# Kernel optimization log

Measured on AMD Instinct MI355X. Metric: run time of the kernel, lower is better.

The kernel has to match this reference:

```python
import jax, jax.numpy as jnp
import numpy as np
import math

N, LQ, C, HD, L, P = 2, 17821, 256, 8, 4, 4
D = C // HD
SHAPES = [(100, 134), (50, 67), (25, 34), (13, 17)]


def setup_inputs() -> dict:
    key = jax.random.key(0)
    ks = jax.random.split(key, 8)
    shapes = np.array(SHAPES, np.int32)
    areas = shapes[:, 0] * shapes[:, 1]
    starts = np.concatenate([[0], np.cumsum(areas)[:-1]]).astype(np.int32)
    Lin = int(areas.sum())
    sc = 1.0 / math.sqrt(C)
    # sampling_offsets bias: radial grid init as in _reset_parameters
    thetas = np.arange(HD, dtype=np.float32) * (2.0 * math.pi / HD)
    grid = np.stack([np.cos(thetas), np.sin(thetas)], -1)
    grid = grid / np.abs(grid).max(-1, keepdims=True)
    grid = np.tile(grid[:, None, None, :], (1, L, P, 1)) * np.arange(1, P + 1, dtype=np.float32)[None, None, :, None]
    boff = jnp.asarray(grid.reshape(-1), jnp.float32)
    return dict(
        query=jax.random.normal(ks[0], (N, LQ, C), jnp.float32),
        reference_points=jax.random.uniform(ks[1], (N, LQ, L, 2), jnp.float32),
        input_flatten=jax.random.normal(ks[2], (N, Lin, C), jnp.float32),
        input_spatial_shapes=jnp.asarray(shapes),
        input_level_start_index=jnp.asarray(starts),
        Wv=jax.random.normal(ks[3], (C, C), jnp.float32) * sc,
        bv=jnp.zeros((C,), jnp.float32),
        Woff=jax.random.normal(ks[4], (C, HD * L * P * 2), jnp.float32) * 0.01,
        boff=boff,
        Watt=jax.random.normal(ks[5], (C, HD * L * P), jnp.float32) * 0.02,
        batt=jnp.zeros((HD * L * P,), jnp.float32),
        Wout=jax.random.normal(ks[6], (C, C), jnp.float32) * sc,
        bout=jnp.zeros((C,), jnp.float32),
    )


def _ms_deform_attn_core(value, shapes, starts, loc, attw):
    # value: (N, Len_in, HD, D); loc: (N, Lq, HD, L, P, 2) in [0,1]; attw: (N, Lq, HD, L, P)
    n, lq = loc.shape[0], loc.shape[1]
    out = jnp.zeros((n, lq, HD, D), value.dtype)
    for l in range(L):
        H, W = int(shapes[l, 0]), int(shapes[l, 1])
        s = int(starts[l])
        v = value[:, s:s + H * W]                                    # (N, HW, HD, D)
        # (N,Lq,HD,P,2) -> (N,Lq,P,HD,2) -> (N,Lq*P,HD) per coord
        locl = loc[:, :, :, l].transpose(0, 1, 3, 2, 4).reshape(n, lq * P, HD, 2)
        # grid_sample align_corners=False mapping
        x = locl[..., 0] * W - 0.5
        y = locl[..., 1] * H - 0.5
        x0f, y0f = jnp.floor(x), jnp.floor(y)
        fx, fy = x - x0f, y - y0f
        x0, y0 = x0f.astype(jnp.int32), y0f.astype(jnp.int32)

        def corner(xi, yi, w):
            valid = (xi >= 0) & (xi < W) & (yi >= 0) & (yi < H)      # zero padding
            idx = jnp.clip(yi, 0, H - 1) * W + jnp.clip(xi, 0, W - 1)
            g = jnp.take_along_axis(v, idx[..., None], axis=1)        # (N, Lq*P, HD, D)
            return g * (w * valid)[..., None]

        samp = (corner(x0, y0, (1 - fx) * (1 - fy))
                + corner(x0 + 1, y0, fx * (1 - fy))
                + corner(x0, y0 + 1, (1 - fx) * fy)
                + corner(x0 + 1, y0 + 1, fx * fy))                    # (N, Lq*P, HD, D)
        aw = attw[:, :, :, l].transpose(0, 1, 3, 2).reshape(n, lq * P, HD)
        out = out + (samp * aw[..., None]).reshape(n, lq, P, HD, D).sum(axis=2)
    return out.reshape(n, lq, HD * D)


def reference(query, reference_points, input_flatten, input_spatial_shapes,
              input_level_start_index, Wv, bv, Woff, boff, Watt, batt, Wout, bout):
    shapes = np.asarray(input_spatial_shapes)
    starts = np.asarray(input_level_start_index)
    n, lq, _ = query.shape
    value = (input_flatten @ Wv + bv).reshape(n, -1, HD, D)
    offsets = (query @ Woff + boff).reshape(n, lq, HD, L, P, 2)
    # reference_points has last dim 2 -> normalize offsets by (W, H) per level
    norm = jnp.asarray(shapes[:, ::-1], jnp.float32)                  # (L, 2) = (W, H)
    loc = reference_points[:, :, None, :, None, :] + offsets / norm[None, None, None, :, None, :]
    attw = (query @ Watt + batt).reshape(n, lq, HD, L * P)
    attw = jax.nn.softmax(attw, axis=-1).reshape(n, lq, HD, L, P)
    out = _ms_deform_attn_core(value, shapes, starts, loc, attw)
    return out @ Wout + bout
```

## Files before the change

### kernel.cpp

```cpp
#include <hip/hip_runtime.h>
#include <hip/hip_bf16.h>
#include <math.h>

#define NB    2
#define LQ    17821
#define LIN   17821
#define CCH   256
#define HDN   8
#define DCH   32
#define LVL   4
#define NPT   4
#define KDIM  256

__constant__ const int   cH[LVL]  = {100, 50, 25, 13};
__constant__ const int   cW[LVL]  = {134, 67, 34, 17};
__constant__ const int   cS[LVL]  = {0, 13400, 16750, 17600};
__constant__ const float cHf[LVL] = {100.f, 50.f, 25.f, 13.f};
__constant__ const float cWf[LVL] = {134.f, 67.f, 34.f, 17.f};
__constant__ const float cRH[LVL] = {1.f/100.f, 1.f/50.f, 1.f/25.f, 1.f/13.f};
__constant__ const float cRW[LVL] = {1.f/134.f, 1.f/67.f, 1.f/34.f, 1.f/17.f};

typedef __attribute__((ext_vector_type(8))) _Float16 f16x8;
typedef __attribute__((ext_vector_type(4))) _Float16 f16x4;
typedef __attribute__((ext_vector_type(4))) float    f32x4;

__device__ __forceinline__ void glds16(const void* g, void* l) {
    __builtin_amdgcn_global_load_lds(
        (const __attribute__((address_space(1))) void*)g,
        (__attribute__((address_space(3))) void*)l, 16, 0, 0);
}

__global__ void prep_all(const float* __restrict__ Wv,
                         const float* __restrict__ Woff,
                         const float* __restrict__ Watt,
                         const float* __restrict__ Wout,
                         const float* __restrict__ boff,
                         const float* __restrict__ batt,
                         _Float16* __restrict__ wvT,
                         _Float16* __restrict__ wqT,
                         _Float16* __restrict__ wuT,
                         float* __restrict__ b384)
{
    const int i = blockIdx.x * 256 + threadIdx.x;
    if (i < 65536) {
        const int n = i >> 8, k = i & 255;
        wvT[i] = (_Float16)Wv[(size_t)k * 256 + n];
    } else if (i < 131072) {
        const int j = i - 65536, n = j >> 8, k = j & 255;
        wqT[j] = (_Float16)Woff[(size_t)k * 256 + n];
    } else if (i < 163840) {
        const int j = i - 131072, n = j >> 8, k = j & 255;
        wqT[65536 + j] = (_Float16)Watt[(size_t)k * 128 + n];
    } else if (i < 229376) {
        const int j = i - 163840, n = j >> 8, k = j & 255;
        wuT[j] = (_Float16)Wout[(size_t)k * 256 + n];
    } else {
        const int j = i - 229376;
        if (j < 256)      b384[j] = boff[j];
        else if (j < 384) b384[j] = batt[j - 256];
    }
}

__global__ void cvt_a(const float* __restrict__ X, _Float16* __restrict__ Y, int n4)
{
    const int stride = gridDim.x * 256;
    for (int i = blockIdx.x * 256 + threadIdx.x; i < n4; i += stride) {
        const float4 v = reinterpret_cast<const float4*>(X)[i];
        f16x4 h;
        h[0] = (_Float16)v.x; h[1] = (_Float16)v.y;
        h[2] = (_Float16)v.z; h[3] = (_Float16)v.w;
        reinterpret_cast<f16x4*>(Y)[i] = h;
    }
}

template<typename OutT>
__global__ __launch_bounds__(256, 2) void gemm_tile(
    const _Float16* __restrict__ A,
    const _Float16* __restrict__ BT,
    const float* __restrict__ bias, OutT* __restrict__ C,
    int M, int Ntot)
{
    __shared__ _Float16 As[2][4096];
    __shared__ _Float16 Bs[2][4096];

    const int t    = threadIdx.x;
    const int wav  = t >> 6;
    const int lane = t & 63;
    const int bm   = blockIdx.y * 128;
    const int bn   = blockIdx.x * 128;

    const int wr = wav >> 1, wc = wav & 1;
    const int fcol = lane & 15;
    const int fk   = lane >> 4;

    int aoff[4], boff[4];
#pragma unroll
    for (int i = 0; i < 4; ++i) {
        const int ar = wr * 64 + i * 16 + fcol;
        aoff[i] = ar * 64 + ((fk ^ ((ar >> 1) & 3)) << 4);
        const int br = wc * 64 + i * 16 + fcol;
        boff[i] = br * 64 + ((fk ^ ((br >> 1) & 3)) << 4);
    }

    const int srow = lane >> 2;
    const int skb  = (lane & 3) << 4;

    f32x4 acc[4][4];
#pragma unroll
    for (int i = 0; i < 4; ++i)
#pragma unroll
        for (int j = 0; j < 4; ++j) acc[i][j] = (f32x4)(0.f);

    auto stage = [&](int s, int buf) {
        const int k0b = s * 64;
#pragma unroll
        for (int i = 0; i < 2; ++i) {
            const int j   = wav + i * 4;
            const int row = j * 16 + srow;
            const int kb  = skb ^ (((row >> 1) & 3) << 4);
            const int rga = min(bm + row, M - 1);
            glds16((const char*)A + (size_t)rga * 512 + k0b + kb,
                   (char*)As[buf] + j * 1024);
            const int rgb = bn + row;
            glds16((const char*)BT + (size_t)rgb * 512 + k0b + kb,
                   (char*)Bs[buf] + j * 1024);
        }
    };

    stage(0, 0);
    __syncthreads();
    int cur = 0;
#pragma unroll 1
    for (int s = 0; s < 8; ++s) {
        if (s + 1 < 8) stage(s + 1, cur ^ 1);
        f16x8 af[4], bfr[4];
#pragma unroll
        for (int i = 0; i < 4; ++i) {
            af[i]  = *reinterpret_cast<const f16x8*>((const char*)As[cur] + aoff[i]);
            bfr[i] = *reinterpret_cast<const f16x8*>((const char*)Bs[cur] + boff[i]);
        }
#pragma unroll
        for (int mi = 0; mi < 4; ++mi)
#pragma unroll
            for (int ni = 0; ni < 4; ++ni)
                acc[mi][ni] = __builtin_amdgcn_mfma_f32_16x16x32_f16(
                    af[mi], bfr[ni], acc[mi][ni], 0, 0, 0);
        __syncthreads();
        cur ^= 1;
    }

    const int r0 = bm + wr * 64 + (lane >> 4) * 4;
    const int c0 = bn + wc * 64 + fcol;
#pragma unroll
    for (int ni = 0; ni < 4; ++ni) {
        const float bv = bias[c0 + ni * 16];
#pragma unroll
        for (int mi = 0; mi < 4; ++mi) {
#pragma unroll
            for (int j = 0; j < 4; ++j) {
                const int r = r0 + mi * 16 + j;
                if (r < M) C[(size_t)r * Ntot + c0 + ni * 16] = (OutT)(acc[mi][ni][j] + bv);
            }
        }
    }
}

__global__ __launch_bounds__(256) void msda_sample(
    const _Float16* __restrict__ value,
    const float* __restrict__ qproj,
    const float* __restrict__ refp,
    _Float16* __restrict__ o16)
{
    __shared__ int   sIdx[2][HDN][16][4];
    __shared__ float sWgt[2][HDN][16][4];

    const int t = threadIdx.x;

    {
        const int qs = t >> 7;
        const int h  = (t >> 4) & 7;
        const int ip = t & 15;
        const int l  = ip >> 2;

        const int r = blockIdx.x * 2 + qs;
        const int n = r / LQ;
        const float* qrow = qproj + (size_t)r * 384;

        const float logit = qrow[256 + h * 16 + ip];
        float m = logit;
#pragma unroll
        for (int k = 8; k >= 1; k >>= 1) m = fmaxf(m, __shfl_xor(m, k));
        const float e = __expf(logit - m);
        float s = e;
#pragma unroll
        for (int k = 8; k >= 1; k >>= 1) s += __shfl_xor(s, k);
        const float aw = e / s;

        const float ox = qrow[h * 32 + ip * 2 + 0];
        const float oy = qrow[h * 32 + ip * 2 + 1];
        const float rx = refp[(size_t)r * 8 + l * 2 + 0];
        const float ry = refp[(size_t)r * 8 + l * 2 + 1];

        const int   Ww = cW[l], Hh = cH[l], st = cS[l];
        const float Wf = cWf[l], Hf = cHf[l];
        const float rW = cRW[l], rH = cRH[l];

        const float x = (rx + ox * rW) * Wf - 0.5f;
        const float y = (ry + oy * rH) * Hf - 0.5f;
        const float x0f = floorf(x);
        const float y0f = floorf(y);
        const float fx = x - x0f;
        const float fy = y - y0f;
        const int x0 = (int)x0f, y0 = (int)y0f;
        const int x1 = x0 + 1,   y1 = y0 + 1;

        const bool vx0 = (x0 >= 0) & (x0 < Ww);
        const bool vx1 = (x1 >= 0) & (x1 < Ww);
        const bool vy0 = (y0 >= 0) & (y0 < Hh);
        const bool vy1 = (y1 >= 0) & (y1 < Hh);

        const float gx0 = 1.f - fx, gx1 = fx;
        const float gy0 = 1.f - fy, gy1 = fy;

        const float w00 = (vx0 & vy0) ? gx0 * gy0 * aw : 0.f;
        const float w10 = (vx1 & vy0) ? gx1 * gy0 * aw : 0.f;
        const float w01 = (vx0 & vy1) ? gx0 * gy1 * aw : 0.f;
        const float w11 = (vx1 & vy1) ? gx1 * gy1 * aw : 0.f;

        const int xc0 = min(max(x0, 0), Ww - 1);
        const int xc1 = min(max(x1, 0), Ww - 1);
        const int yc0 = min(max(y0, 0), Hh - 1);
        const int yc1 = min(max(y1, 0), Hh - 1);

        const int base = (n * LIN + st) * CCH + h * DCH;
        sIdx[qs][h][ip][0] = (base + (yc0 * Ww + xc0) * CCH) * 2;
        sIdx[qs][h][ip][1] = (base + (yc0 * Ww + xc1) * CCH) * 2;
        sIdx[qs][h][ip][2] = (base + (yc1 * Ww + xc0) * CCH) * 2;
        sIdx[qs][h][ip][3] = (base + (yc1 * Ww + xc1) * CCH) * 2;
        sWgt[qs][h][ip][0] = w00;
        sWgt[qs][h][ip][1] = w10;
        sWgt[qs][h][ip][2] = w01;
        sWgt[qs][h][ip][3] = w11;
    }

    __syncthreads();

    const int g   = t >> 5;
    const int w   = t & 31;
    const int sub = w & 3;
    const int c   = (w >> 2) & 3;
    const int p2  = w >> 4;
    const char* vbase = (const char*)value + sub * 16;

    float acc0[8] = {}, acc1[8] = {};

#pragma unroll
    for (int i8 = 0; i8 < 8; ++i8) {
        const int ip = i8 * 2 + p2;
        const int   id0 = sIdx[0][g][ip][c];
        const float wt0 = sWgt[0][g][ip][c];
        const int   id1 = sIdx[1][g][ip][c];
        const float wt1 = sWgt[1][g][ip][c];
        const f16x8 v0 = *reinterpret_cast<const f16x8*>(vbase + id0);
        const f16x8 v1 = *reinterpret_cast<const f16x8*>(vbase + id1);
#pragma unroll
        for (int j = 0; j < 8; ++j) {
            acc0[j] = fmaf((float)v0[j], wt0, acc0[j]);
            acc1[j] = fmaf((float)v1[j], wt1, acc1[j]);
        }
    }

#pragma unroll
    for (int k = 4; k <= 16; k <<= 1) {
#pragma unroll
        for (int j = 0; j < 8; ++j) {
            acc0[j] += __shfl_xor(acc0[j], k);
            acc1[j] += __shfl_xor(acc1[j], k);
        }
    }

    if (w < 4) {
        const int r0 = blockIdx.x * 2;
        const size_t o = (size_t)r0 * 256 + g * 32 + sub * 8;
        f16x8 h0, h1;
#pragma unroll
        for (int j = 0; j < 8; ++j) {
            h0[j] = (_Float16)acc0[j];
            h1[j] = (_Float16)acc1[j];
        }
        *reinterpret_cast<f16x8*>(&o16[o])       = h0;
        *reinterpret_cast<f16x8*>(&o16[o + 256]) = h1;
    }
}

extern "C" void kernel_launch(void* const* d_in, const int* in_sizes, int n_in,
                              void* d_out, int out_size, void* d_ws, size_t ws_size,
                              hipStream_t stream)
{
    const float* query  = (const float*)d_in[0];
    const float* refp   = (const float*)d_in[1];
    const float* inflat = (const float*)d_in[2];
    const float* Wv     = (const float*)d_in[5];
    const float* bv     = (const float*)d_in[6];
    const float* Woff   = (const float*)d_in[7];
    const float* boff   = (const float*)d_in[8];
    const float* Watt   = (const float*)d_in[9];
    const float* batt   = (const float*)d_in[10];
    const float* Wout   = (const float*)d_in[11];
    const float* bout   = (const float*)d_in[12];
    float* out = (float*)d_out;

    const int M = NB * LQ;
    const size_t MC = (size_t)M * 256;

    float* ws    = (float*)d_ws;
    float* qproj = ws;
    float* b384  = qproj + (size_t)M * 384;

    _Float16* fbase = (_Float16*)(b384 + 384);
    _Float16* ih16  = fbase;
    _Float16* qh16  = ih16 + MC;
    _Float16* v16   = qh16 + MC;
    _Float16* o16   = v16 + MC;
    _Float16* wvT   = o16 + MC;
    _Float16* wqT   = wvT + 65536;
    _Float16* wuT   = wqT + 98304;

    const dim3 blk(256);
    const int mblk = (M + 127) / 128;
    const int n4   = (int)(MC / 4);

    prep_all<<<dim3(898), blk, 0, stream>>>(Wv, Woff, Watt, Wout, boff, batt,
                                            wvT, wqT, wuT, b384);

    cvt_a<<<dim3(2048), blk, 0, stream>>>(inflat, ih16, n4);
    cvt_a<<<dim3(2048), blk, 0, stream>>>(query,  qh16, n4);

    gemm_tile<_Float16><<<dim3(2, mblk), blk, 0, stream>>>(ih16, wvT, bv,   v16,   M, 256);
    gemm_tile<float><<<dim3(3, mblk), blk, 0, stream>>>(qh16, wqT, b384, qproj, M, 384);

    msda_sample<<<dim3(M / 2), blk, 0, stream>>>(v16, qproj, refp, o16);

    gemm_tile<float><<<dim3(2, mblk), blk, 0, stream>>>(o16, wuT, bout, out, M, 256);
}
```

Measured before the change: 183.3 us.

## Store value head-major, query projections in fp16, fuse conversions, pack index/weight

The value GEMM now writes its output in a per-(batch, head) contiguous layout, so each head's 32 channels of all positions sit together, which should improve gather locality in the sampling kernel. The offset/attention projection is stored as fp16 instead of fp32 to halve that traffic. The two fp32-to-fp16 conversion launches are merged into one kernel, and sampling indices and weights are packed into a single int2 shared array. The permuted epilogue scatters GEMM stores less contiguously, and fp16 offsets/logits reduce the precision of the sampling locations.

```diff
diff --git a/kernel.cpp b/kernel.cpp
--- a/kernel.cpp
+++ b/kernel.cpp
@@ -61,19 +61,22 @@
     }
 }
 
-__global__ void cvt_a(const float* __restrict__ X, _Float16* __restrict__ Y, int n4)
+__global__ void cvt_two(const float* __restrict__ X0, const float* __restrict__ X1,
+                        _Float16* __restrict__ Y0, _Float16* __restrict__ Y1, int n4)
 {
     const int stride = gridDim.x * 256;
-    for (int i = blockIdx.x * 256 + threadIdx.x; i < n4; i += stride) {
-        const float4 v = reinterpret_cast<const float4*>(X)[i];
+    for (int i = blockIdx.x * 256 + threadIdx.x; i < 2 * n4; i += stride) {
+        const bool second = i >= n4;
+        const int j = second ? i - n4 : i;
+        const float4 v = reinterpret_cast<const float4*>(second ? X1 : X0)[j];
         f16x4 h;
         h[0] = (_Float16)v.x; h[1] = (_Float16)v.y;
         h[2] = (_Float16)v.z; h[3] = (_Float16)v.w;
-        reinterpret_cast<f16x4*>(Y)[i] = h;
-    }
-}
-
-template<typename OutT>
+        reinterpret_cast<f16x4*>(second ? Y1 : Y0)[j] = h;
+    }
+}
+
+template<typename OutT, bool PERM>
 __global__ __launch_bounds__(256, 2) void gemm_tile(
     const _Float16* __restrict__ A,
     const _Float16* __restrict__ BT,
@@ -153,13 +156,24 @@
     const int c0 = bn + wc * 64 + fcol;
 #pragma unroll
     for (int ni = 0; ni < 4; ++ni) {
-        const float bv = bias[c0 + ni * 16];
+        const int col = c0 + ni * 16;
+        const float bv = bias[col];
 #pragma unroll
         for (int mi = 0; mi < 4; ++mi) {
 #pragma unroll
             for (int j = 0; j < 4; ++j) {
                 const int r = r0 + mi * 16 + j;
-                if (r < M) C[(size_t)r * Ntot + c0 + ni * 16] = (OutT)(acc[mi][ni][j] + bv);
+                if (r < M) {
+                    const float v = acc[mi][ni][j] + bv;
+                    if (PERM) {
+                        const int n   = (r >= LIN) ? 1 : 0;
+                        const int pos = r - n * LIN;
+                        const size_t dst = ((size_t)(n * HDN + (col >> 5)) * LIN + pos) * 32 + (col & 31);
+                        C[dst] = (OutT)v;
+                    } else {
+                        C[(size_t)r * Ntot + col] = (OutT)v;
+                    }
+                }
             }
         }
     }
@@ -167,12 +181,11 @@
 
 __global__ __launch_bounds__(256) void msda_sample(
     const _Float16* __restrict__ value,
-    const float* __restrict__ qproj,
+    const _Float16* __restrict__ qproj,
     const float* __restrict__ refp,
     _Float16* __restrict__ o16)
 {
-    __shared__ int   sIdx[2][HDN][16][4];
-    __shared__ float sWgt[2][HDN][16][4];
+    __shared__ int2 sIW[2][HDN][16][4];
 
     const int t = threadIdx.x;
 
@@ -184,9 +197,9 @@
 
         const int r = blockIdx.x * 2 + qs;
         const int n = r / LQ;
-        const float* qrow = qproj + (size_t)r * 384;
-
-        const float logit = qrow[256 + h * 16 + ip];
+        const _Float16* qrow = qproj + (size_t)r * 384;
+
+        const float logit = (float)qrow[256 + h * 16 + ip];
         float m = logit;
 #pragma unroll
         for (int k = 8; k >= 1; k >>= 1) m = fmaxf(m, __shfl_xor(m, k));
@@ -196,8 +209,8 @@
         for (int k = 8; k >= 1; k >>= 1) s += __shfl_xor(s, k);
         const float aw = e / s;
 
-        const float ox = qrow[h * 32 + ip * 2 + 0];
-        const float oy = qrow[h * 32 + ip * 2 + 1];
+        const float ox = (float)qrow[h * 32 + ip * 2 + 0];
+        const float oy = (float)qrow[h * 32 + ip * 2 + 1];
         const float rx = refp[(size_t)r * 8 + l * 2 + 0];
         const float ry = refp[(size_t)r * 8 + l * 2 + 1];
 
@@ -232,15 +245,11 @@
         const int yc0 = min(max(y0, 0), Hh - 1);
         const int yc1 = min(max(y1, 0), Hh - 1);
 
-        const int base = (n * LIN + st) * CCH + h * DCH;
-        sIdx[qs][h][ip][0] = (base + (yc0 * Ww + xc0) * CCH) * 2;
-        sIdx[qs][h][ip][1] = (base + (yc0 * Ww + xc1) * CCH) * 2;
-        sIdx[qs][h][ip][2] = (base + (yc1 * Ww + xc0) * CCH) * 2;
-        sIdx[qs][h][ip][3] = (base + (yc1 * Ww + xc1) * CCH) * 2;
-        sWgt[qs][h][ip][0] = w00;
-        sWgt[qs][h][ip][1] = w10;
-        sWgt[qs][h][ip][2] = w01;
-        sWgt[qs][h][ip][3] = w11;
+        const int base = (n * HDN + h) * LIN + st;
+        sIW[qs][h][ip][0] = make_int2((base + yc0 * Ww + xc0) * 64, __float_as_int(w00));
+        sIW[qs][h][ip][1] = make_int2((base + yc0 * Ww + xc1) * 64, __float_as_int(w10));
+        sIW[qs][h][ip][2] = make_int2((base + yc1 * Ww + xc0) * 64, __float_as_int(w01));
+        sIW[qs][h][ip][3] = make_int2((base + yc1 * Ww + xc1) * 64, __float_as_int(w11));
     }
 
     __syncthreads();
@@ -257,12 +266,12 @@
 #pragma unroll
     for (int i8 = 0; i8 < 8; ++i8) {
         const int ip = i8 * 2 + p2;
-        const int   id0 = sIdx[0][g][ip][c];
-        const float wt0 = sWgt[0][g][ip][c];
-        const int   id1 = sIdx[1][g][ip][c];
-        const float wt1 = sWgt[1][g][ip][c];
-        const f16x8 v0 = *reinterpret_cast<const f16x8*>(vbase + id0);
-        const f16x8 v1 = *reinterpret_cast<const f16x8*>(vbase + id1);
+        const int2 iw0 = sIW[0][g][ip][c];
+        const int2 iw1 = sIW[1][g][ip][c];
+        const float wt0 = __int_as_float(iw0.y);
+        const float wt1 = __int_as_float(iw1.y);
+        const f16x8 v0 = *reinterpret_cast<const f16x8*>(vbase + iw0.x);
+        const f16x8 v1 = *reinterpret_cast<const f16x8*>(vbase + iw1.x);
 #pragma unroll
         for (int j = 0; j < 8; ++j) {
             acc0[j] = fmaf((float)v0[j], wt0, acc0[j]);
@@ -313,12 +322,12 @@
     const int M = NB * LQ;
     const size_t MC = (size_t)M * 256;
 
-    float* ws    = (float*)d_ws;
-    float* qproj = ws;
-    float* b384  = qproj + (size_t)M * 384;
+    float* ws   = (float*)d_ws;
+    float* b384 = ws;
 
     _Float16* fbase = (_Float16*)(b384 + 384);
-    _Float16* ih16  = fbase;
+    _Float16* qp16  = fbase;
+    _Float16* ih16  = qp16 + (size_t)M * 384;
     _Float16* qh16  = ih16 + MC;
     _Float16* v16   = qh16 + MC;
     _Float16* o16   = v16 + MC;
@@ -333,13 +342,12 @@
     prep_all<<<dim3(898), blk, 0, stream>>>(Wv, Woff, Watt, Wout, boff, batt,
                                             wvT, wqT, wuT, b384);
 
-    cvt_a<<<dim3(2048), blk, 0, stream>>>(inflat, ih16, n4);
-    cvt_a<<<dim3(2048), blk, 0, stream>>>(query,  qh16, n4);
-
-    gemm_tile<_Float16><<<dim3(2, mblk), blk, 0, stream>>>(ih16, wvT, bv,   v16,   M, 256);
-    gemm_tile<float><<<dim3(3, mblk), blk, 0, stream>>>(qh16, wqT, b384, qproj, M, 384);
-
-    msda_sample<<<dim3(M / 2), blk, 0, stream>>>(v16, qproj, refp, o16);
-
-    gemm_tile<float><<<dim3(2, mblk), blk, 0, stream>>>(o16, wuT, bout, out, M, 256);
-}
+    cvt_two<<<dim3(2048), blk, 0, stream>>>(inflat, query, ih16, qh16, n4);
+
+    gemm_tile<_Float16, true><<<dim3(2, mblk), blk, 0, stream>>>(ih16, wvT, bv, v16, M, 256);
+    gemm_tile<_Float16, false><<<dim3(3, mblk), blk, 0, stream>>>(qh16, wqT, b384, qp16, M, 384);
+
+    msda_sample<<<dim3(M / 2), blk, 0, stream>>>(v16, qp16, refp, o16);
+
+    gemm_tile<float, false><<<dim3(2, mblk), blk, 0, stream>>>(o16, wuT, bout, out, M, 256);
+}
```

Measured after the change: 178.3 us. 1.03x faster.
